# Optimization experiments

Hardware: AMD Instinct MI355X
Metric: run time of the kernel (lower is better)

The kernel has to match this reference:

```python
import jax, jax.numpy as jnp
import numpy as np

EPS_NORM = 1e-12
EPS_COS = 1e-8

def _l2norm(x, axis):
    n = jnp.linalg.norm(x, axis=axis, keepdims=True)
    return x / jnp.maximum(n, EPS_NORM)

def setup_inputs() -> dict:
    key = jax.random.key(0)
    k1, k2, k3 = jax.random.split(key, 3)
    B, C, H, W, M = 16, 512, 32, 32, 1024
    query = jax.random.normal(k1, (B, C, H, W), dtype=jnp.float32)
    keys = jax.random.normal(k2, (M, C), dtype=jnp.float32)
    entropy = jax.random.uniform(k3, (B * H * W, 1), dtype=jnp.float32) + 1e-3
    return {"query": query, "keys": keys, "entropy": entropy}

def reference(query, keys, entropy):
    B, C, H, W = query.shape
    M = keys.shape[0]
    N = B * H * W
    # F.normalize over channel dim, then BCHW -> BHWC -> [N, C]
    q = _l2norm(query, axis=1)
    q = jnp.transpose(q, (0, 2, 3, 1))
    qr = q.reshape(N, C)

    # get_score: softmax over queries (axis 0) and over memory (axis 1)
    score = jnp.einsum('nd,md->nm', qr, keys)  # [N, M]
    sq = jax.nn.softmax(score, axis=0)
    sm = jax.nn.softmax(score, axis=1)

    # ---- memory_loss ----
    argm = jnp.argmax(sm, axis=1)               # topk(k=1) over memory
    closest = keys[argm]                         # [N, C]
    eye = jnp.eye(M, dtype=keys.dtype)
    gram = keys @ keys.T
    diversity_loss = jnp.sum((gram * (1.0 - eye)) ** 2) / (M * M - M)
    cos = jnp.sum(qr * closest, axis=1) / jnp.maximum(
        jnp.linalg.norm(qr, axis=1) * jnp.linalg.norm(closest, axis=1), EPS_COS)
    similarity_loss = jnp.dot(1.0 - cos, entropy[:, 0])  # CosineEmbeddingLoss(target=1) . entropy

    # ---- read ----
    concat_memory = jax.lax.stop_gradient(sm) @ keys    # [N, C]
    updated_query = jnp.concatenate([qr, concat_memory], axis=1)  # [N, 2C]
    updated_query = updated_query.reshape(B, H, W, 2 * C)
    updated_query = jnp.transpose(updated_query, (0, 3, 1, 2))    # [B, 2C, H, W]

    # ---- update (train=True) ----
    g = argm                                     # gathering indices (argmax == topk1)
    sq_d = jax.lax.stop_gradient(sq)
    ent_d = jax.lax.stop_gradient(entropy[:, 0])
    colmax = jnp.max(sq_d, axis=0)               # max score per memory slot [M]
    w = (sq_d[jnp.arange(N), g] / colmax[g]) * (ent_d / jnp.max(ent_d))  # [N]
    query_update = jax.ops.segment_sum(w[:, None] * qr, g, num_segments=M)  # [M, C]
    updated_memory = _l2norm(query_update + jax.lax.stop_gradient(keys), axis=1)
    gram2 = updated_memory @ updated_memory.T
    diversity_loss_updated = jnp.sum((gram2 * (1.0 - eye)) ** 2) / (M * M - M)
    updated_memory = jax.lax.stop_gradient(updated_memory)

    return (updated_query, updated_memory, sq, sm, diversity_loss_updated, similarity_loss)
```

## Files before the change

### kernel.cpp

```cpp
#include <hip/hip_runtime.h>

typedef unsigned int  u32;
typedef unsigned short u16;
typedef __bf16 bf16x8 __attribute__((ext_vector_type(8)));
typedef float  f32x4  __attribute__((ext_vector_type(4)));

#define O1 16777216
#define O2 17301504
#define O3 34078720
#define O4 50855936
#define O5 50855937

#define WS_QHI   0u
#define WS_QLO   16777216u
#define WS_KHI   33554432u
#define WS_KLO   34603008u
#define WS_KT    35651584u
#define WS_KNORM 36700160u
#define WS_CNT   36704256u
#define WS_OFFS  36708352u
#define WS_CUR   36712704u
#define WS_RN    36769792u
#define WS_PMAX  36835328u
#define WS_CMAX  36966400u
#define WS_CSUM  36970496u
#define WS_ARGM  36974592u
#define WS_WGT   37040128u
#define WS_EMAX  37199872u
#define WS_SCAL  39202816u
#define WS_PM2   39203840u
#define WS_PS2   39728128u
#define WS_SM16  40252416u

__device__ __forceinline__ u16 bf_rne(float f){
  u32 u = __float_as_uint(f);
  u32 r = u + 0x7fffu + ((u >> 16) & 1u);
  return (u16)(r >> 16);
}
__device__ __forceinline__ float bf_f(u16 h){ return __uint_as_float(((u32)h) << 16); }

__device__ __forceinline__ void glds16(const void* g, void* l){
  __builtin_amdgcn_global_load_lds((const __attribute__((address_space(1))) u32*)g,
                                   (__attribute__((address_space(3))) u32*)l, 16, 0, 0);
}

__global__ __launch_bounds__(256) void k_pre(
    const float* __restrict__ keys, const float* __restrict__ ent,
    const float* __restrict__ query, float* __restrict__ out0,
    u16* __restrict__ khi, u16* __restrict__ klo, float* __restrict__ knorm,
    u16* __restrict__ kT, float* __restrict__ emax,
    u16* __restrict__ qhi, u16* __restrict__ qlo, float* __restrict__ rn_g){
  __shared__ float shmem[64*65 + 256 + 64];
  float* tile = shmem;
  float* red  = shmem + 64*65;
  float* sinv = red + 256;
  int bx = blockIdx.x; int t = threadIdx.x;

  if (bx < 256){
    int wave = t >> 6, l = t & 63;
    int m = bx*4 + wave;
    const float* kr = keys + (size_t)m*512 + l*8;
    float f[8];
    #pragma unroll
    for (int i=0;i<8;i++) f[i] = kr[i];
    float ss = 0.f;
    #pragma unroll
    for (int i=0;i<8;i++) ss += f[i]*f[i];
    for (int o=32;o>0;o>>=1) ss += __shfl_xor(ss,o);
    if (l == 0) knorm[m] = sqrtf(ss);
    u32 hh[4], ll[4];
    #pragma unroll
    for (int i=0;i<4;i++){
      u16 h0 = bf_rne(f[2*i]);   u16 l0 = bf_rne(f[2*i]   - bf_f(h0));
      u16 h1 = bf_rne(f[2*i+1]); u16 l1 = bf_rne(f[2*i+1] - bf_f(h1));
      hh[i] = (u32)h0 | ((u32)h1<<16);
      ll[i] = (u32)l0 | ((u32)l1<<16);
    }
    *(uint4*)&khi[(size_t)m*512 + l*8] = make_uint4(hh[0],hh[1],hh[2],hh[3]);
    *(uint4*)&klo[(size_t)m*512 + l*8] = make_uint4(ll[0],ll[1],ll[2],ll[3]);
  } else if (bx < 384){
    int g = bx - 256;
    int m0 = (g & 15)*64, c0 = (g >> 4)*64;
    int j = t & 63; int ig = t >> 6;
    #pragma unroll 4
    for (int ii=0; ii<16; ++ii){
      int i = ig*16 + ii;
      tile[i*65 + j] = keys[(size_t)(m0+i)*512 + c0 + j];
    }
    __syncthreads();
    #pragma unroll 4
    for (int ii=0; ii<16; ++ii){
      int i = ig*16 + ii;
      kT[(size_t)(c0+i)*1024 + m0 + j] = bf_rne(tile[j*65 + i]);
    }
  } else if (bx < 416){
    int g = bx - 384;
    int i = g*512 + t;
    float v = fmaxf(ent[i], ent[i + 256]);
    for (int o=32;o>0;o>>=1) v = fmaxf(v, __shfl_xor(v,o));
    if ((t & 63) == 0) red[t>>6] = v;
    __syncthreads();
    if (t == 0) emax[g] = fmaxf(fmaxf(red[0],red[1]), fmaxf(red[2],red[3]));
  } else {
    int bx2 = bx - 416;
    int b = bx2 >> 4; int hw0 = (bx2 & 15)*64;
    int hw = t & 63; int cg = t >> 6;
    const float* qb = query + (size_t)b*524288 + hw0 + hw;
    float p = 0.f;
    for (int c = cg; c < 512; c += 4){ float v = qb[(size_t)c*1024]; p += v*v; }
    red[cg*64 + hw] = p;
    __syncthreads();
    if (t < 64){
      float ss = red[t] + red[64+t] + red[128+t] + red[192+t];
      float nrm = sqrtf(ss);
      float inv = 1.0f / fmaxf(nrm, 1e-12f);
      sinv[t] = inv;
      rn_g[b*1024 + hw0 + t] = nrm * inv;
    }
    __syncthreads();
    int nl = t >> 2, cq = t & 3;
    int n = b*1024 + hw0 + nl;
    float invv = sinv[hw];
    for (int cb = 0; cb < 8; ++cb){
      int cbase = cb*64;
      #pragma unroll 4
      for (int i = 0; i < 16; ++i){
        int cl = cg*16 + i;
        int c = cbase + cl;
        float v = query[(size_t)b*524288 + (size_t)c*1024 + hw0 + hw] * invv;
        tile[cl*65 + hw] = v;
        out0[(size_t)b*1048576 + (size_t)c*1024 + hw0 + hw] = v;
      }
      __syncthreads();
      u32 hh[8], ll[8];
      #pragma unroll
      for (int p2 = 0; p2 < 8; ++p2){
        float f0 = tile[(cq*16 + p2*2)*65 + nl];
        float f1 = tile[(cq*16 + p2*2 + 1)*65 + nl];
        u16 h0 = bf_rne(f0); u16 lo0 = bf_rne(f0 - bf_f(h0));
        u16 h1 = bf_rne(f1); u16 lo1 = bf_rne(f1 - bf_f(h1));
        hh[p2] = (u32)h0 | ((u32)h1 << 16);
        ll[p2] = (u32)lo0 | ((u32)lo1 << 16);
      }
      size_t base = (size_t)n*512 + cbase + cq*16;
      *(uint4*)&qhi[base]     = make_uint4(hh[0],hh[1],hh[2],hh[3]);
      *(uint4*)&qhi[base + 8] = make_uint4(hh[4],hh[5],hh[6],hh[7]);
      *(uint4*)&qlo[base]     = make_uint4(ll[0],ll[1],ll[2],ll[3]);
      *(uint4*)&qlo[base + 8] = make_uint4(ll[4],ll[5],ll[6],ll[7]);
      __syncthreads();
    }
  }
}

__global__ __launch_bounds__(256) void k_score(const u16* __restrict__ qhi, const u16* __restrict__ qlo,
    const u16* __restrict__ khi, const u16* __restrict__ klo, float* __restrict__ S,
    float* __restrict__ pm2, float* __restrict__ ps2){
  __shared__ u16 sAh[8192], sAl[8192], sBh[8192], sBl[8192];
  int tid = threadIdx.x;
  int wg = ((blockIdx.x & 7) << 7) + (blockIdx.x >> 3);
  int nt = wg >> 3, mt = wg & 7;
  int nBase = nt*128, mBase = mt*128;
  int wave = tid >> 6, lane = tid & 63;
  int rw = (wave>>1)*64, cw = (wave&1)*64;
  int m16 = lane & 15, q4 = lane >> 4;
  f32x4 acc[4][4] = {};
  int srow = tid >> 3, sg = tid & 7;
  for (int kit = 0; kit < 8; ++kit){
    int k0 = kit*64;
    #pragma unroll
    for (int it = 0; it < 4; ++it){
      int row = it*32 + srow;
      int gsw = (sg ^ (row & 7)) * 8;
      int lo = it*2048 + tid*8;
      glds16(qhi + (size_t)(nBase + row)*512 + k0 + gsw, &sAh[lo]);
      glds16(qlo + (size_t)(nBase + row)*512 + k0 + gsw, &sAl[lo]);
      glds16(khi + (size_t)(mBase + row)*512 + k0 + gsw, &sBh[lo]);
      glds16(klo + (size_t)(mBase + row)*512 + k0 + gsw, &sBl[lo]);
    }
    __syncthreads();
    #pragma unroll
    for (int ks = 0; ks < 2; ++ks){
      bf16x8 a0[4], a1[4], b0[4], b1[4];
      int g = ks*4 + q4;
      #pragma unroll
      for (int i=0;i<4;i++){
        int r = rw + i*16 + m16;
        int off = r*64 + (g ^ (r&7))*8;
        a0[i] = *(const bf16x8*)&sAh[off];
        a1[i] = *(const bf16x8*)&sAl[off];
      }
      #pragma unroll
      for (int j=0;j<4;j++){
        int r = cw + j*16 + m16;
        int off = r*64 + (g ^ (r&7))*8;
        b0[j] = *(const bf16x8*)&sBh[off];
        b1[j] = *(const bf16x8*)&sBl[off];
      }
      #pragma unroll
      for (int i=0;i<4;i++)
        #pragma unroll
        for (int j=0;j<4;j++){
          acc[i][j] = __builtin_amdgcn_mfma_f32_16x16x32_bf16(a0[i], b0[j], acc[i][j], 0,0,0);
          acc[i][j] = __builtin_amdgcn_mfma_f32_16x16x32_bf16(a0[i], b1[j], acc[i][j], 0,0,0);
          acc[i][j] = __builtin_amdgcn_mfma_f32_16x16x32_bf16(a1[i], b0[j], acc[i][j], 0,0,0);
        }
    }
    __syncthreads();
  }
  #pragma unroll
  for (int i=0;i<4;i++){
    int rbase = nBase + rw + i*16 + q4*4;
    #pragma unroll
    for (int j=0;j<4;j++){
      int col = mBase + cw + j*16 + m16;
      #pragma unroll
      for (int r=0;r<4;r++)
        S[(size_t)(rbase + r)*1024 + col] = acc[i][j][r];
    }
  }
  float* lm = (float*)sAh;
  float* ls = lm + 256;
  #pragma unroll
  for (int j=0;j<4;j++){
    float cm = -3.4e38f;
    #pragma unroll
    for (int i=0;i<4;i++)
      #pragma unroll
      for (int r=0;r<4;r++) cm = fmaxf(cm, acc[i][j][r]);
    cm = fmaxf(cm, __shfl_xor(cm, 16));
    cm = fmaxf(cm, __shfl_xor(cm, 32));
    float cs = 0.f;
    #pragma unroll
    for (int i=0;i<4;i++)
      #pragma unroll
      for (int r=0;r<4;r++) cs += __expf(acc[i][j][r] - cm);
    cs += __shfl_xor(cs, 16);
    cs += __shfl_xor(cs, 32);
    if (lane < 16){
      lm[(wave*4 + j)*16 + m16] = cm;
      ls[(wave*4 + j)*16 + m16] = cs;
    }
  }
  __syncthreads();
  if (tid < 128){
    int w = tid >> 6;
    int x = tid & 63;
    int j = x >> 4, c16 = x & 15;
    float m0 = lm[(w*4 + j)*16 + c16],     s0 = ls[(w*4 + j)*16 + c16];
    float m1 = lm[((w+2)*4 + j)*16 + c16], s1 = ls[((w+2)*4 + j)*16 + c16];
    float M  = fmaxf(m0, m1);
    float Sv = s0*__expf(m0 - M) + s1*__expf(m1 - M);
    int col = mBase + w*64 + j*16 + c16;
    pm2[nt*1024 + col] = M;
    ps2[nt*1024 + col] = Sv;
  }
}

__global__ __launch_bounds__(256) void k_colfin(const float* __restrict__ pm2, const float* __restrict__ ps2,
    float* __restrict__ cmax, float* __restrict__ csum,
    const float* __restrict__ emax, float* __restrict__ scal, u32* __restrict__ count){
  int bx = blockIdx.x, t = threadIdx.x;
  if (bx < 4) count[bx*256 + t] = 0u;
  if (bx == 4 && t == 0){
    float mx = emax[0];
    for (int i=1;i<32;i++) mx = fmaxf(mx, emax[i]);
    scal[0] = 0.f; scal[1] = mx; scal[2] = 0.f; scal[3] = 0.f;
  }
  int col = bx*64 + (t & 63);
  int grp = t >> 6;
  float M = -3.4e38f, s = 0.f;
  for (int ch = grp*32; ch < grp*32 + 32; ++ch){
    float mi = pm2[ch*1024 + col], si = ps2[ch*1024 + col];
    float nm = fmaxf(M, mi);
    s = s*__expf(M - nm) + si*__expf(mi - nm);
    M = nm;
  }
  __shared__ float gm[256], gs[256];
  gm[t] = M; gs[t] = s;
  __syncthreads();
  if (t < 64){
    float MM = gm[t], ss2 = gs[t];
    #pragma unroll
    for (int g2=1; g2<4; ++g2){
      float mi = gm[g2*64 + t], si = gs[g2*64 + t];
      float nm = fmaxf(MM, mi);
      ss2 = ss2*__expf(MM - nm) + si*__expf(mi - nm);
      MM = nm;
    }
    cmax[col] = MM; csum[col] = ss2;
  }
}

__global__ __launch_bounds__(256) void k_row(float* __restrict__ S, float* __restrict__ sm,
    u16* __restrict__ sm16,
    const float* __restrict__ cmax, const float* __restrict__ csum,
    const float* __restrict__ rn, const float* __restrict__ knorm,
    const float* __restrict__ ent, const float* __restrict__ scal,
    int* __restrict__ argm, float* __restrict__ wgt, u32* __restrict__ count,
    float* __restrict__ sim_acc){
  int wave = threadIdx.x >> 6, lane = threadIdx.x & 63;
  int n = blockIdx.x*4 + wave;
  float4 v[4];
  const float4* Sr = (const float4*)(S + (size_t)n*1024);
  #pragma unroll
  for (int j=0;j<4;j++) v[j] = Sr[j*64 + lane];
  float m = -3.4e38f; int gi = 0;
  #pragma unroll
  for (int j=0;j<4;j++){
    int c0 = j*256 + lane*4;
    if (v[j].x > m){ m=v[j].x; gi=c0; }
    if (v[j].y > m){ m=v[j].y; gi=c0+1; }
    if (v[j].z > m){ m=v[j].z; gi=c0+2; }
    if (v[j].w > m){ m=v[j].w; gi=c0+3; }
  }
  for (int o=32;o>0;o>>=1){
    float om = __shfl_xor(m,o); int oi = __shfl_xor(gi,o);
    if (om > m || (om == m && oi < gi)){ m = om; gi = oi; }
  }
  float4 e[4]; float s = 0.f;
  #pragma unroll
  for (int j=0;j<4;j++){
    e[j].x = __expf(v[j].x - m); e[j].y = __expf(v[j].y - m);
    e[j].z = __expf(v[j].z - m); e[j].w = __expf(v[j].w - m);
    s += e[j].x + e[j].y + e[j].z + e[j].w;
  }
  for (int o=32;o>0;o>>=1) s += __shfl_xor(s,o);
  float ri = 1.f/s;
  float4* smr = (float4*)(sm + (size_t)n*1024);
  #pragma unroll
  for (int j=0;j<4;j++){
    float4 t2; t2.x=e[j].x*ri; t2.y=e[j].y*ri; t2.z=e[j].z*ri; t2.w=e[j].w*ri;
    smr[j*64 + lane] = t2;
    u32 w0 = (u32)bf_rne(t2.x) | ((u32)bf_rne(t2.y) << 16);
    u32 w1 = (u32)bf_rne(t2.z) | ((u32)bf_rne(t2.w) << 16);
    *(uint2*)&sm16[(size_t)n*1024 + j*256 + lane*4] = make_uint2(w0, w1);
  }
  float4* sqr = (float4*)(S + (size_t)n*1024);
  #pragma unroll
  for (int j=0;j<4;j++){
    int c0 = j*256 + lane*4;
    float4 cm = *(const float4*)(cmax + c0);
    float4 cs = *(const float4*)(csum + c0);
    float4 q;
    q.x = __expf(v[j].x - cm.x)/cs.x;
    q.y = __expf(v[j].y - cm.y)/cs.y;
    q.z = __expf(v[j].z - cm.z)/cs.z;
    q.w = __expf(v[j].w - cm.w)/cs.w;
    sqr[j*64 + lane] = q;
  }
  __shared__ float simw[4];
  if (lane == 0){
    float en = ent[n];
    float cosv = m / fmaxf(rn[n]*knorm[gi], 1e-8f);
    simw[wave] = (1.f - cosv)*en;
    float w = __expf(m - cmax[gi]) * en / scal[1];
    wgt[n] = w; argm[n] = gi;
    atomicAdd(&count[gi], 1u);
  }
  __syncthreads();
  if (threadIdx.x == 0)
    atomicAdd(sim_acc, simw[0]+simw[1]+simw[2]+simw[3]);
}

__global__ __launch_bounds__(256) void k_scan(const u32* __restrict__ count,
    u32* __restrict__ offs, u32* __restrict__ cursor){
  int t = threadIdx.x;
  u32 v0 = count[t*4], v1 = count[t*4+1], v2 = count[t*4+2], v3 = count[t*4+3];
  u32 s = v0+v1+v2+v3;
  u32 x = s;
  for (int o=1;o<64;o<<=1){ u32 y = __shfl_up(x,o); if ((t&63) >= o) x += y; }
  __shared__ u32 wsum[4];
  if ((t&63) == 63) wsum[t>>6] = x;
  __syncthreads();
  u32 wb = 0;
  for (int wv=0; wv < (t>>6); ++wv) wb += wsum[wv];
  u32 excl = wb + x - s;
  u32 o0 = excl, o1 = excl+v0, o2 = excl+v0+v1, o3 = excl+v0+v1+v2;
  offs[t*4]=o0; offs[t*4+1]=o1; offs[t*4+2]=o2; offs[t*4+3]=o3;
  cursor[t*4]=o0; cursor[t*4+1]=o1; cursor[t*4+2]=o2; cursor[t*4+3]=o3;
  if (t == 255) offs[1024] = 16384u;
}

__global__ __launch_bounds__(256) void k_bucket(const int* __restrict__ argm,
    u32* __restrict__ cursor, u32* __restrict__ list){
  int n = blockIdx.x*256 + threadIdx.x;
  int g = argm[n];
  u32 pos = atomicAdd(&cursor[g], 1u);
  list[pos] = n;
}

__global__ __launch_bounds__(128) void k_gather(const u16* __restrict__ qhi, const u16* __restrict__ qlo,
    const u32* __restrict__ offs, const u32* __restrict__ list, const float* __restrict__ wgt,
    const float* __restrict__ keys, float* __restrict__ out1, float* __restrict__ scal){
  int m = blockIdx.x, t = threadIdx.x;
  int c0 = t*4;
  float a0=0.f,a1=0.f,a2=0.f,a3=0.f;
  u32 beg = offs[m], end = offs[m+1];
  for (u32 r = beg; r < end; ++r){
    int n = (int)list[r];
    float w = wgt[n];
    uint2 hh = *(const uint2*)&qhi[(size_t)n*512 + c0];
    uint2 ll = *(const uint2*)&qlo[(size_t)n*512 + c0];
    float f0 = bf_f((u16)(hh.x & 0xffffu)) + bf_f((u16)(ll.x & 0xffffu));
    float f1 = bf_f((u16)(hh.x >> 16))     + bf_f((u16)(ll.x >> 16));
    float f2 = bf_f((u16)(hh.y & 0xffffu)) + bf_f((u16)(ll.y & 0xffffu));
    float f3 = bf_f((u16)(hh.y >> 16))     + bf_f((u16)(ll.y >> 16));
    a0 += w*f0; a1 += w*f1; a2 += w*f2; a3 += w*f3;
  }
  float4 k4 = *(const float4*)(keys + (size_t)m*512 + c0);
  float u0 = a0 + k4.x, u1 = a1 + k4.y, u2 = a2 + k4.z, u3 = a3 + k4.w;
  float ss = u0*u0 + u1*u1 + u2*u2 + u3*u3;
  for (int o=32;o>0;o>>=1) ss += __shfl_xor(ss,o);
  __shared__ float r2[2];
  if ((t&63) == 0) r2[t>>6] = ss;
  __syncthreads();
  float tot = r2[0] + r2[1];
  float inv = 1.f / fmaxf(sqrtf(tot), 1e-12f);
  float4 o4; o4.x=u0*inv; o4.y=u1*inv; o4.z=u2*inv; o4.w=u3*inv;
  *(float4*)(out1 + (size_t)m*512 + c0) = o4;
  if (t == 0){
    float s2 = tot*inv*inv;
    atomicAdd(scal + 3, s2*s2);
  }
}

__global__ __launch_bounds__(256) void k_concat(const u16* __restrict__ kT, const u16* __restrict__ sm16,
    float* __restrict__ out0){
  __shared__ u16 sA[8192];
  __shared__ u16 sB[8192];
  int tid = threadIdx.x;
  int wg = ((blockIdx.x & 7) << 6) + (blockIdx.x >> 3);
  int ct = wg & 3, nt = wg >> 2;
  int cBase = ct*128, nBase = nt*128;
  int wave = tid>>6, lane = tid&63;
  int rw = (wave>>1)*64, cw = (wave&1)*64;
  int m16 = lane&15, q4 = lane>>4;
  f32x4 acc[4][4] = {};
  int srow = tid>>3, sg = tid&7;
  for (int kit=0; kit<16; ++kit){
    int k0 = kit*64;
    #pragma unroll
    for (int it=0; it<4; ++it){
      int row = it*32 + srow;
      int gsw = (sg ^ (row & 7)) * 8;
      int lo = it*2048 + tid*8;
      glds16(kT   + (size_t)(cBase + row)*1024 + k0 + gsw, &sA[lo]);
      glds16(sm16 + (size_t)(nBase + row)*1024 + k0 + gsw, &sB[lo]);
    }
    __syncthreads();
    #pragma unroll
    for (int ks=0; ks<2; ++ks){
      bf16x8 a[4], b[4];
      int g = ks*4 + q4;
      #pragma unroll
      for (int i=0;i<4;i++){
        int r = rw + i*16 + m16;
        a[i] = *(const bf16x8*)&sA[r*64 + (g ^ (r&7))*8];
      }
      #pragma unroll
      for (int j=0;j<4;j++){
        int r = cw + j*16 + m16;
        b[j] = *(const bf16x8*)&sB[r*64 + (g ^ (r&7))*8];
      }
      #pragma unroll
      for (int i=0;i<4;i++)
        #pragma unroll
        for (int j=0;j<4;j++)
          acc[i][j] = __builtin_amdgcn_mfma_f32_16x16x32_bf16(a[i], b[j], acc[i][j], 0,0,0);
    }
    __syncthreads();
  }
  #pragma unroll
  for (int i=0;i<4;i++){
    int c = cBase + rw + i*16 + q4*4;
    #pragma unroll
    for (int j=0;j<4;j++){
      int n = nBase + cw + j*16 + m16;
      int b2 = n >> 10, hw = n & 1023;
      #pragma unroll
      for (int r=0;r<4;r++)
        out0[(size_t)b2*1048576 + (size_t)(512 + c + r)*1024 + hw] = acc[i][j][r];
    }
  }
}

__global__ __launch_bounds__(256) void k_gram(const float* __restrict__ U, float* __restrict__ scal){
  __shared__ float Ua[64*34], Ub[64*34];
  int bx = blockIdx.x & 15, by = blockIdx.x >> 4;
  int t = threadIdx.x;
  int c1 = (t >> 4)*2, c2 = (t & 15)*2;
  float d00=0,d01=0,d10=0,d11=0;
  for (int ch=0; ch<16; ++ch){
    #pragma unroll
    for (int j=0;j<8;j++){
      int flat = j*256 + t;
      int ml = flat >> 5, c = flat & 31;
      Ua[ml*34 + c] = U[(size_t)(ch*64 + ml)*512 + bx*32 + c];
      Ub[ml*34 + c] = U[(size_t)(ch*64 + ml)*512 + by*32 + c];
    }
    __syncthreads();
    #pragma unroll 8
    for (int ml=0; ml<64; ++ml){
      float2 a = *(const float2*)&Ua[ml*34 + c1];
      float2 b = *(const float2*)&Ub[ml*34 + c2];
      d00 += a.x*b.x; d01 += a.x*b.y; d10 += a.y*b.x; d11 += a.y*b.y;
    }
    __syncthreads();
  }
  float loc = d00*d00 + d01*d01 + d10*d10 + d11*d11;
  for (int o=32;o>0;o>>=1) loc += __shfl_xor(loc,o);
  __shared__ float r4[4];
  if ((t&63) == 0) r4[t>>6] = loc;
  __syncthreads();
  if (t == 0) atomicAdd(scal + 2, r4[0]+r4[1]+r4[2]+r4[3]);
}

__global__ void k_final(const float* __restrict__ scal, float* __restrict__ out){
  out[O4] = (scal[2] - scal[3]) * (1.0f/1047552.0f);
  out[O5] = scal[0];
}

extern "C" void kernel_launch(void* const* d_in, const int* in_sizes, int n_in,
                              void* d_out, int out_size, void* d_ws, size_t ws_size,
                              hipStream_t stream) {
  const float* query = (const float*)d_in[0];
  const float* keys  = (const float*)d_in[1];
  const float* ent   = (const float*)d_in[2];
  float* out  = (float*)d_out;
  char*  ws   = (char*)d_ws;

  u16*   qhi   = (u16*)(ws + WS_QHI);
  u16*   qlo   = (u16*)(ws + WS_QLO);
  u16*   khi   = (u16*)(ws + WS_KHI);
  u16*   klo   = (u16*)(ws + WS_KLO);
  u16*   kT    = (u16*)(ws + WS_KT);
  float* knorm = (float*)(ws + WS_KNORM);
  u32*   count = (u32*)(ws + WS_CNT);
  u32*   offs  = (u32*)(ws + WS_OFFS);
  u32*   cursor= (u32*)(ws + WS_CUR);
  float* rn    = (float*)(ws + WS_RN);
  float* cmax  = (float*)(ws + WS_CMAX);
  float* csum  = (float*)(ws + WS_CSUM);
  int*   argm  = (int*)(ws + WS_ARGM);
  float* wgt   = (float*)(ws + WS_WGT);
  float* emax  = (float*)(ws + WS_EMAX);
  float* scal  = (float*)(ws + WS_SCAL);
  u32*   list  = (u32*)(ws + WS_PMAX);
  float* pm2   = (float*)(ws + WS_PM2);
  float* ps2   = (float*)(ws + WS_PS2);
  u16*   sm16  = (u16*)(ws + WS_SM16);

  float* S   = out + O2;
  float* sm  = out + O3;
  float* um  = out + O1;

  k_pre    <<<672,  256, 0, stream>>>(keys, ent, query, out, khi, klo, knorm, kT, emax, qhi, qlo, rn);
  k_score  <<<1024, 256, 0, stream>>>(qhi, qlo, khi, klo, S, pm2, ps2);
  k_colfin <<<16,   256, 0, stream>>>(pm2, ps2, cmax, csum, emax, scal, count);
  k_row    <<<4096, 256, 0, stream>>>(S, sm, sm16, cmax, csum, rn, knorm, ent, scal, argm, wgt, count, scal );
  k_scan   <<<1,    256, 0, stream>>>(count, offs, cursor);
  k_bucket <<<64,   256, 0, stream>>>(argm, cursor, list);
  k_gather <<<1024, 128, 0, stream>>>(qhi, qlo, offs, list, wgt, keys, um, scal);
  k_concat <<<512,  256, 0, stream>>>(kT, sm16, out);
  k_gram   <<<256,  256, 0, stream>>>(um, scal);
  k_final  <<<1,      1, 0, stream>>>(scal, out);
}
```

Baseline: 489.4 us.

## Double-buffer LDS tiles in score and concat GEMM kernels

Both MFMA GEMM kernels now split their LDS tiles into two buffers with half the K depth (32 instead of 64). The global-to-LDS copy for the next K slice is issued before computing on the current one, with one barrier per iteration instead of two. This is meant to overlap global memory latency with MFMA work. In exchange it doubles the number of iterations and barriers and uses a new XOR swizzle for the narrower rows. The MFMA calls in the score kernel are also regrouped into three passes.

```diff
diff --git a/kernel.cpp b/kernel.cpp
--- a/kernel.cpp
+++ b/kernel.cpp
@@ -164,47 +164,58 @@
   int rw = (wave>>1)*64, cw = (wave&1)*64;
   int m16 = lane & 15, q4 = lane >> 4;
   f32x4 acc[4][4] = {};
-  int srow = tid >> 3, sg = tid & 7;
-  for (int kit = 0; kit < 8; ++kit){
-    int k0 = kit*64;
-    #pragma unroll
-    for (int it = 0; it < 4; ++it){
-      int row = it*32 + srow;
-      int gsw = (sg ^ (row & 7)) * 8;
-      int lo = it*2048 + tid*8;
-      glds16(qhi + (size_t)(nBase + row)*512 + k0 + gsw, &sAh[lo]);
-      glds16(qlo + (size_t)(nBase + row)*512 + k0 + gsw, &sAl[lo]);
-      glds16(khi + (size_t)(mBase + row)*512 + k0 + gsw, &sBh[lo]);
-      glds16(klo + (size_t)(mBase + row)*512 + k0 + gsw, &sBl[lo]);
-    }
-    __syncthreads();
-    #pragma unroll
-    for (int ks = 0; ks < 2; ++ks){
-      bf16x8 a0[4], a1[4], b0[4], b1[4];
-      int g = ks*4 + q4;
-      #pragma unroll
-      for (int i=0;i<4;i++){
-        int r = rw + i*16 + m16;
-        int off = r*64 + (g ^ (r&7))*8;
-        a0[i] = *(const bf16x8*)&sAh[off];
-        a1[i] = *(const bf16x8*)&sAl[off];
-      }
-      #pragma unroll
-      for (int j=0;j<4;j++){
-        int r = cw + j*16 + m16;
-        int off = r*64 + (g ^ (r&7))*8;
-        b0[j] = *(const bf16x8*)&sBh[off];
-        b1[j] = *(const bf16x8*)&sBl[off];
-      }
-      #pragma unroll
-      for (int i=0;i<4;i++)
-        #pragma unroll
-        for (int j=0;j<4;j++){
-          acc[i][j] = __builtin_amdgcn_mfma_f32_16x16x32_bf16(a0[i], b0[j], acc[i][j], 0,0,0);
-          acc[i][j] = __builtin_amdgcn_mfma_f32_16x16x32_bf16(a0[i], b1[j], acc[i][j], 0,0,0);
-          acc[i][j] = __builtin_amdgcn_mfma_f32_16x16x32_bf16(a1[i], b0[j], acc[i][j], 0,0,0);
-        }
-    }
+
+  int row2 = tid >> 2;
+  int cg4  = tid & 3;
+  auto STAGE = [&](int d, int kk){
+    int k0 = kk*32;
+    #pragma unroll
+    for (int it=0; it<2; ++it){
+      int row = it*64 + row2;
+      int gs = cg4 ^ ((row >> 1) & 3);
+      size_t ka = (size_t)k0 + gs*8;
+      int lo = d*4096 + it*2048 + tid*8;
+      glds16(qhi + (size_t)(nBase + row)*512 + ka, &sAh[lo]);
+      glds16(qlo + (size_t)(nBase + row)*512 + ka, &sAl[lo]);
+      glds16(khi + (size_t)(mBase + row)*512 + ka, &sBh[lo]);
+      glds16(klo + (size_t)(mBase + row)*512 + ka, &sBl[lo]);
+    }
+  };
+  STAGE(0, 0);
+  __syncthreads();
+  for (int kit = 0; kit < 16; ++kit){
+    int cur = kit & 1;
+    if (kit < 15) STAGE(cur^1, kit+1);
+    bf16x8 a0[4], a1[4], b0[4], b1[4];
+    #pragma unroll
+    for (int i=0;i<4;i++){
+      int r = rw + i*16 + m16;
+      int off = cur*4096 + r*32 + (q4 ^ ((r>>1)&3))*8;
+      a0[i] = *(const bf16x8*)&sAh[off];
+      a1[i] = *(const bf16x8*)&sAl[off];
+    }
+    #pragma unroll
+    for (int j=0;j<4;j++){
+      int r = cw + j*16 + m16;
+      int off = cur*4096 + r*32 + (q4 ^ ((r>>1)&3))*8;
+      b0[j] = *(const bf16x8*)&sBh[off];
+      b1[j] = *(const bf16x8*)&sBl[off];
+    }
+    #pragma unroll
+    for (int i=0;i<4;i++)
+      #pragma unroll
+      for (int j=0;j<4;j++)
+        acc[i][j] = __builtin_amdgcn_mfma_f32_16x16x32_bf16(a0[i], b0[j], acc[i][j], 0,0,0);
+    #pragma unroll
+    for (int i=0;i<4;i++)
+      #pragma unroll
+      for (int j=0;j<4;j++)
+        acc[i][j] = __builtin_amdgcn_mfma_f32_16x16x32_bf16(a0[i], b1[j], acc[i][j], 0,0,0);
+    #pragma unroll
+    for (int i=0;i<4;i++)
+      #pragma unroll
+      for (int j=0;j<4;j++)
+        acc[i][j] = __builtin_amdgcn_mfma_f32_16x16x32_bf16(a1[i], b0[j], acc[i][j], 0,0,0);
     __syncthreads();
   }
   #pragma unroll
@@ -436,38 +447,42 @@
   int rw = (wave>>1)*64, cw = (wave&1)*64;
   int m16 = lane&15, q4 = lane>>4;
   f32x4 acc[4][4] = {};
-  int srow = tid>>3, sg = tid&7;
-  for (int kit=0; kit<16; ++kit){
-    int k0 = kit*64;
-    #pragma unroll
-    for (int it=0; it<4; ++it){
-      int row = it*32 + srow;
-      int gsw = (sg ^ (row & 7)) * 8;
-      int lo = it*2048 + tid*8;
-      glds16(kT   + (size_t)(cBase + row)*1024 + k0 + gsw, &sA[lo]);
-      glds16(sm16 + (size_t)(nBase + row)*1024 + k0 + gsw, &sB[lo]);
-    }
-    __syncthreads();
-    #pragma unroll
-    for (int ks=0; ks<2; ++ks){
-      bf16x8 a[4], b[4];
-      int g = ks*4 + q4;
-      #pragma unroll
-      for (int i=0;i<4;i++){
-        int r = rw + i*16 + m16;
-        a[i] = *(const bf16x8*)&sA[r*64 + (g ^ (r&7))*8];
-      }
-      #pragma unroll
-      for (int j=0;j<4;j++){
-        int r = cw + j*16 + m16;
-        b[j] = *(const bf16x8*)&sB[r*64 + (g ^ (r&7))*8];
-      }
-      #pragma unroll
-      for (int i=0;i<4;i++)
-        #pragma unroll
-        for (int j=0;j<4;j++)
-          acc[i][j] = __builtin_amdgcn_mfma_f32_16x16x32_bf16(a[i], b[j], acc[i][j], 0,0,0);
-    }
+
+  int row2 = tid >> 2;
+  int cg4  = tid & 3;
+  auto STAGE = [&](int d, int kk){
+    int k0 = kk*32;
+    #pragma unroll
+    for (int it=0; it<2; ++it){
+      int row = it*64 + row2;
+      int gs = cg4 ^ ((row >> 1) & 3);
+      size_t ka = (size_t)k0 + gs*8;
+      int lo = d*4096 + it*2048 + tid*8;
+      glds16(kT   + (size_t)(cBase + row)*1024 + ka, &sA[lo]);
+      glds16(sm16 + (size_t)(nBase + row)*1024 + ka, &sB[lo]);
+    }
+  };
+  STAGE(0, 0);
+  __syncthreads();
+  for (int kit=0; kit<32; ++kit){
+    int cur = kit & 1;
+    if (kit < 31) STAGE(cur^1, kit+1);
+    bf16x8 a[4], b[4];
+    #pragma unroll
+    for (int i=0;i<4;i++){
+      int r = rw + i*16 + m16;
+      a[i] = *(const bf16x8*)&sA[cur*4096 + r*32 + (q4 ^ ((r>>1)&3))*8];
+    }
+    #pragma unroll
+    for (int j=0;j<4;j++){
+      int r = cw + j*16 + m16;
+      b[j] = *(const bf16x8*)&sB[cur*4096 + r*32 + (q4 ^ ((r>>1)&3))*8];
+    }
+    #pragma unroll
+    for (int i=0;i<4;i++)
+      #pragma unroll
+      for (int j=0;j<4;j++)
+        acc[i][j] = __builtin_amdgcn_mfma_f32_16x16x32_bf16(a[i], b[j], acc[i][j], 0,0,0);
     __syncthreads();
   }
   #pragma unroll
```

After: 508.7 us. +4.0%, slower.
